# Optimization experiments

Measured on AMD Instinct MI355X. Metric: run time of the kernel, lower is better.

The kernel has to match this reference:

```python
import jax, jax.numpy as jnp
import numpy as np

N = 100000   # nodes
E = 1600000  # edges (avg degree 16)
F = 128      # num_features
H = 128      # hidden
BN_EPS = 1e-5
NORM_EPS = 1e-12


def setup_inputs() -> dict:
    key = jax.random.key(0)
    k = jax.random.split(key, 5)
    x = jax.random.normal(k[0], (N, F), dtype=jnp.float32)
    edge_index = jax.random.randint(k[1], (2, E), 0, N, dtype=jnp.int64)
    # Xavier-uniform linear weights (as in weights_init)
    s = float(np.sqrt(6.0 / (F + H)))
    W_l = jax.random.uniform(k[2], (F, H), jnp.float32, -s, s)  # neighbor branch
    b_l = jnp.zeros((H,), jnp.float32)
    W_r = jax.random.uniform(k[3], (F, H), jnp.float32, -s, s)  # root branch (no bias in PyG)
    gamma = jnp.ones((H,), jnp.float32)   # BatchNorm weight
    beta = jnp.zeros((H,), jnp.float32)   # BatchNorm bias
    return {"x": x, "edge_index": edge_index, "W_l": W_l, "b_l": b_l,
            "W_r": W_r, "gamma": gamma, "beta": beta}


def reference(x, edge_index, W_l, b_l, W_r, gamma, beta):
    n = x.shape[0]
    src, dst = edge_index[0], edge_index[1]
    # mean aggregation of neighbor messages x_j at destination nodes
    agg = jax.ops.segment_sum(x[src], dst, num_segments=n)                 # [N, F]
    deg = jax.ops.segment_sum(jnp.ones((src.shape[0],), x.dtype), dst,
                              num_segments=n)                              # [N]
    agg = agg / jnp.maximum(deg, 1.0)[:, None]
    # SAGEConv: lin_l(agg) + lin_r(x), then row-wise L2 normalize
    out = agg @ W_l + b_l + x @ W_r                                        # [N, H]
    nrm = jnp.sqrt(jnp.sum(out * out, axis=-1, keepdims=True))
    out = out / jnp.maximum(nrm, NORM_EPS)
    # transition: ReLU -> BatchNorm1d (batch stats, training mode) -> Dropout(identity)
    out = jax.nn.relu(out)
    mean = jnp.mean(out, axis=0)
    var = jnp.mean((out - mean) ** 2, axis=0)  # biased variance (torch BN)
    out = (out - mean) / jnp.sqrt(var + BN_EPS) * gamma + beta
    return out
```

## Files before the change

kernel.cpp:

```cpp
#include <hip/hip_runtime.h>
#include <hip/hip_bf16.h>

static constexpr int F = 128;
static constexpr int H = 128;
static constexpr int NPART = 128;

typedef __attribute__((ext_vector_type(8))) short short8;
typedef __attribute__((ext_vector_type(4))) float f32x4;

__device__ __forceinline__ unsigned short f2bf(float f) {
  union { float f; unsigned u; } a; a.f = f;
  unsigned r = a.u + 0x7FFF + ((a.u >> 16) & 1);
  return (unsigned short)(r >> 16);
}
__device__ __forceinline__ float bf2f(unsigned short h) {
  union { unsigned u; float f; } a; a.u = ((unsigned)h) << 16;
  return a.f;
}
__device__ __forceinline__ float bits2f(unsigned u) {
  union { unsigned u; float f; } a; a.u = u;
  return a.f;
}

__device__ __forceinline__ unsigned f2fp8(float f) {
  union { float f; unsigned u; } a; a.f = f;
  unsigned s = (a.u >> 24) & 0x80u;
  unsigned m = a.u & 0x7FFFFFFFu;
  if (m < 0x3C800000u) return s;
  unsigned r = m + 0x7FFFFu + ((m >> 20) & 1u);
  if (r > 0x43E00000u) r = 0x43E00000u;
  return s | ((((r >> 23) - 120u) & 15u) << 3) | ((r >> 20) & 7u);
}

__device__ __forceinline__ void fp8x4_to_f32(unsigned w, float& f0, float& f1,
                                             float& f2, float& f3) {
  unsigned lo = w & 0x00FF00FFu;
  unsigned hi = (w >> 8) & 0x00FF00FFu;
  unsigned p0 = (((lo << 4) & 0x07F007F0u) + 0x3C003C00u) | ((lo & 0x00800080u) << 8);
  unsigned p1 = (((hi << 4) & 0x07F007F0u) + 0x3C003C00u) | ((hi & 0x00800080u) << 8);
  f0 = bits2f(p0 << 16);
  f2 = bits2f(p0 & 0xFFFF0000u);
  f1 = bits2f(p1 << 16);
  f3 = bits2f(p1 & 0xFFFF0000u);
}

__device__ __forceinline__ int detect64(const void* eiv) {
  const unsigned* u = (const unsigned*)eiv;
  int is64 = 1;
  for (int i = 0; i < 64; ++i) is64 &= (u[2 * i + 1] == 0u);
  return is64;
}

__global__ void detect_dtype(const unsigned* __restrict__ ei, int* __restrict__ flag) {
  if (blockIdx.x == 0 && threadIdx.x == 0) {
    int is64 = 1;
    for (int i = 0; i < 64; ++i) {
      if (ei[2 * i + 1] != 0u) { is64 = 0; break; }
    }
    *flag = is64;
  }
}

__device__ __forceinline__ int load_idx(const void* eiv, int is64, long long pos) {
  return is64 ? (int)((const long long*)eiv)[pos] : ((const int*)eiv)[pos];
}

__global__ __launch_bounds__(512) void part_hist(const void* __restrict__ eiv,
                                                 int* __restrict__ cmat,
                                                 int E, int nbuck, int chunk) {
  __shared__ int h[2048];
  const int t = threadIdx.x, b = blockIdx.x;
  for (int i = t; i < nbuck; i += 512) h[i] = 0;
  __syncthreads();
  int is64 = detect64(eiv);
  int s = b * chunk, e = min(E, s + chunk);
  for (int i = s + t; i < e; i += 512) {
    int dst = load_idx(eiv, is64, (long long)E + i);
    atomicAdd(&h[dst >> 6], 1);
  }
  __syncthreads();
  for (int i = t; i < nbuck; i += 512) cmat[i * NPART + b] = h[i];
}

__global__ __launch_bounds__(256) void scan1(const int* __restrict__ in,
                                             int* __restrict__ outx,
                                             int* __restrict__ blocksum, int n) {
  __shared__ int sm[256];
  int idx = blockIdx.x * 256 + threadIdx.x;
  int v = (idx < n) ? in[idx] : 0;
  sm[threadIdx.x] = v;
  __syncthreads();
  #pragma unroll
  for (int off = 1; off < 256; off <<= 1) {
    int t = (threadIdx.x >= off) ? sm[threadIdx.x - off] : 0;
    __syncthreads();
    sm[threadIdx.x] += t;
    __syncthreads();
  }
  if (idx < n) outx[idx] = sm[threadIdx.x] - v;
  if (threadIdx.x == 255) blocksum[blockIdx.x] = sm[255];
}

__global__ __launch_bounds__(1024) void scan2big(const int* __restrict__ blocksum,
                                                 int* __restrict__ blockoff, int nb) {
  __shared__ int sm[1024];
  int t = threadIdx.x;
  int v = (t < nb) ? blocksum[t] : 0;
  sm[t] = v;
  __syncthreads();
  for (int off = 1; off < 1024; off <<= 1) {
    int u = (t >= off) ? sm[t - off] : 0;
    __syncthreads();
    sm[t] += u;
    __syncthreads();
  }
  if (t < nb) blockoff[t] = sm[t] - v;
}

__global__ __launch_bounds__(256) void scan3p(int* __restrict__ obuf,
                                              const int* __restrict__ blockoff,
                                              int* __restrict__ bbase,
                                              float* __restrict__ colzero,
                                              int L, int nbuck, int E) {
  if (blockIdx.x == 0) colzero[threadIdx.x] = 0.0f;
  int idx = blockIdx.x * 256 + threadIdx.x;
  if (idx >= L) return;
  int v = obuf[idx] + blockoff[idx >> 8];
  obuf[idx] = v;
  if ((idx & (NPART - 1)) == 0) bbase[idx / NPART] = v;
  if (idx == 0) bbase[nbuck] = E;
}

__global__ __launch_bounds__(512) void part_scatter(const void* __restrict__ eiv,
                                                    const int* __restrict__ base,
                                                    int* __restrict__ ebuf,
                                                    int E, int nbuck, int chunk) {
  __shared__ int cur[2048];
  const int t = threadIdx.x, b = blockIdx.x;
  for (int i = t; i < nbuck; i += 512) cur[i] = base[i * NPART + b];
  __syncthreads();
  int is64 = detect64(eiv);
  int s = b * chunk, e = min(E, s + chunk);
  for (int i = s + t; i < e; i += 512) {
    int src = load_idx(eiv, is64, i);
    int dst = load_idx(eiv, is64, (long long)E + i);
    int pos = atomicAdd(&cur[dst >> 6], 1);
    ebuf[pos] = (src << 6) | (dst & 63);
  }
}

#define GCAP 2048
template <bool LOWP>
__global__ __launch_bounds__(256) void gather_bucket(
    const unsigned char* __restrict__ Yf8, const int* __restrict__ ebuf,
    const int* __restrict__ bbase, float* __restrict__ pio,
    const unsigned short* __restrict__ Pbf, unsigned short* __restrict__ Ubf,
    float* __restrict__ colsum, float* __restrict__ colsq, int n) {
  __shared__ int lsrc[GCAP];
  __shared__ int hist[65];
  __shared__ int loff[65];
  __shared__ int cur[64];
  __shared__ float csm[128], cqm[128];

  const int t = threadIdx.x;
  const int b = blockIdx.x;
  const int node0 = b << 6;
  const int s = bbase[b], e = bbase[b + 1];
  const int cnt = e - s;

  if (t < 65) hist[t] = 0;
  if (t < 128) { csm[t] = 0.f; cqm[t] = 0.f; }
  __syncthreads();

  const bool fast = (cnt <= GCAP);
  if (fast) {
    for (int i = s + t; i < e; i += 256)
      atomicAdd(&hist[ebuf[i] & 63], 1);
    __syncthreads();
    if (t < 64) loff[t] = hist[t];
    __syncthreads();
    #pragma unroll
    for (int off = 1; off < 64; off <<= 1) {
      int u = (t >= off && t < 64) ? loff[t - off] : 0;
      __syncthreads();
      if (t < 64) loff[t] += u;
      __syncthreads();
    }
    if (t < 64) cur[t] = loff[t] - hist[t];
    __syncthreads();
    for (int i = s + t; i < e; i += 256) {
      int p = ebuf[i];
      int pos = atomicAdd(&cur[p & 63], 1);
      lsrc[pos] = p >> 6;
    }
    __syncthreads();
  }

  const int lane = t & 63;
  const int w = t >> 6;
  const int half = lane >> 5;
  const int c = (lane & 31) * 4;

  float lcs[4] = {0.f, 0.f, 0.f, 0.f};
  float lcq[4] = {0.f, 0.f, 0.f, 0.f};

  #pragma unroll
  for (int it = 0; it < 8; ++it) {
    int ln = it * 8 + w * 2 + half;
    int node = node0 + ln;
    if (node >= n) continue;
    int ls, le;
    if (fast) { ls = loff[ln] - hist[ln]; le = loff[ln]; }
    else      { ls = 0; le = 0; }

    float acc[8][4];
    #pragma unroll
    for (int u = 0; u < 8; ++u)
      #pragma unroll
      for (int q = 0; q < 4; ++q) acc[u][q] = 0.0f;

    int j = ls;
    for (; j + 7 < le; j += 8) {
      #pragma unroll
      for (int u = 0; u < 8; ++u) {
        int sj = lsrc[j + u];
        unsigned wv = *(const unsigned*)(Yf8 + (size_t)sj * H + c);
        float f0, f1, f2, f3;
        fp8x4_to_f32(wv, f0, f1, f2, f3);
        acc[u][0] += f0; acc[u][1] += f1; acc[u][2] += f2; acc[u][3] += f3;
      }
    }
    for (; j + 1 < le; j += 2) {
      #pragma unroll
      for (int u = 0; u < 2; ++u) {
        int sj = lsrc[j + u];
        unsigned wv = *(const unsigned*)(Yf8 + (size_t)sj * H + c);
        float f0, f1, f2, f3;
        fp8x4_to_f32(wv, f0, f1, f2, f3);
        acc[u][0] += f0; acc[u][1] += f1; acc[u][2] += f2; acc[u][3] += f3;
      }
    }
    if (j < le) {
      int sj = lsrc[j];
      unsigned wv = *(const unsigned*)(Yf8 + (size_t)sj * H + c);
      float f0, f1, f2, f3;
      fp8x4_to_f32(wv, f0, f1, f2, f3);
      acc[0][0] += f0; acc[0][1] += f1; acc[0][2] += f2; acc[0][3] += f3;
    }

    float deg = 0.0f;
    float a0, a1, a2, a3;
    if (fast) {
      deg = (float)(le - ls);
      #pragma unroll
      for (int u = 4; u < 8; ++u) {
        acc[u - 4][0] += acc[u][0]; acc[u - 4][1] += acc[u][1];
        acc[u - 4][2] += acc[u][2]; acc[u - 4][3] += acc[u][3];
      }
      a0 = (acc[0][0] + acc[1][0]) + (acc[2][0] + acc[3][0]);
      a1 = (acc[0][1] + acc[1][1]) + (acc[2][1] + acc[3][1]);
      a2 = (acc[0][2] + acc[1][2]) + (acc[2][2] + acc[3][2]);
      a3 = (acc[0][3] + acc[1][3]) + (acc[2][3] + acc[3][3]);
    } else {
      a0 = a1 = a2 = a3 = 0.0f;
      for (int jj = s; jj < e; ++jj) {
        int p = ebuf[jj];
        if ((p & 63) == ln) {
          deg += 1.0f;
          unsigned wv = *(const unsigned*)(Yf8 + (size_t)(p >> 6) * H + c);
          float f0, f1, f2, f3;
          fp8x4_to_f32(wv, f0, f1, f2, f3);
          a0 += f0; a1 += f1; a2 += f2; a3 += f3;
        }
      }
    }

    float inv = 1.0f / fmaxf(deg, 1.0f);
    float p0, p1, p2, p3;
    if (LOWP) {
      uint2 pv = *(const uint2*)(Pbf + (size_t)node * H + c);
      p0 = bits2f(pv.x << 16);
      p1 = bits2f(pv.x & 0xFFFF0000u);
      p2 = bits2f(pv.y << 16);
      p3 = bits2f(pv.y & 0xFFFF0000u);
    } else {
      float4 p = *(const float4*)(pio + (size_t)node * H + c);
      p0 = p.x; p1 = p.y; p2 = p.z; p3 = p.w;
    }
    float v0 = p0 + a0 * inv;
    float v1 = p1 + a1 * inv;
    float v2 = p2 + a2 * inv;
    float v3 = p3 + a3 * inv;
    float sq = v0 * v0 + v1 * v1 + v2 * v2 + v3 * v3;
    sq += __shfl_xor(sq, 1, 64);
    sq += __shfl_xor(sq, 2, 64);
    sq += __shfl_xor(sq, 4, 64);
    sq += __shfl_xor(sq, 8, 64);
    sq += __shfl_xor(sq, 16, 64);
    float rs = 1.0f / fmaxf(sqrtf(sq), 1e-12f);
    float u0 = fmaxf(v0 * rs, 0.f), u1 = fmaxf(v1 * rs, 0.f);
    float u2 = fmaxf(v2 * rs, 0.f), u3 = fmaxf(v3 * rs, 0.f);
    if (LOWP) {
      uint2 ov;
      ov.x = (unsigned)f2bf(u0) | ((unsigned)f2bf(u1) << 16);
      ov.y = (unsigned)f2bf(u2) | ((unsigned)f2bf(u3) << 16);
      *(uint2*)(Ubf + (size_t)node * H + c) = ov;
    } else {
      float4 o = {u0, u1, u2, u3};
      *(float4*)(pio + (size_t)node * H + c) = o;
    }
    lcs[0] += u0; lcq[0] += u0 * u0;
    lcs[1] += u1; lcq[1] += u1 * u1;
    lcs[2] += u2; lcq[2] += u2 * u2;
    lcs[3] += u3; lcq[3] += u3 * u3;
  }

  #pragma unroll
  for (int q = 0; q < 4; ++q) {
    atomicAdd(&csm[c + q], lcs[q]);
    atomicAdd(&cqm[c + q], lcq[q]);
  }
  __syncthreads();
  if (t < 128) {
    atomicAdd(&colsum[t], csm[t]);
    atomicAdd(&colsq[t], cqm[t]);
  }
}

__global__ __launch_bounds__(256) void deg_count(const void* __restrict__ eiv,
                                                 const int* __restrict__ flag,
                                                 int* __restrict__ degi, int E) {
  int e = blockIdx.x * blockDim.x + threadIdx.x;
  if (e >= E) return;
  int dst = load_idx(eiv, *flag, (long long)E + e);
  atomicAdd(&degi[dst], 1);
}

__global__ __launch_bounds__(256) void scan3(int* __restrict__ offsets,
                                             const int* __restrict__ blockoff,
                                             int* __restrict__ cursor, int n, int E) {
  int idx = blockIdx.x * 256 + threadIdx.x;
  if (idx >= n) return;
  int off = offsets[idx] + blockoff[idx >> 8];
  offsets[idx] = off;
  cursor[idx] = off;
  if (idx == 0) offsets[n] = E;
}

__global__ __launch_bounds__(256) void bucket_fill(const void* __restrict__ eiv,
                                                   const int* __restrict__ flag,
                                                   int* __restrict__ cursor,
                                                   int* __restrict__ csr_src, int E) {
  int e = blockIdx.x * blockDim.x + threadIdx.x;
  if (e >= E) return;
  int is64 = *flag;
  int src = load_idx(eiv, is64, e);
  int dst = load_idx(eiv, is64, (long long)E + e);
  int pos = atomicAdd(&cursor[dst], 1);
  csr_src[pos] = src;
}

__global__ __launch_bounds__(256) void prep_w(const float* __restrict__ Wl,
                                              const float* __restrict__ Wr,
                                              unsigned short* __restrict__ Wcat) {
  int tid = blockIdx.x * 256 + threadIdx.x;
  if (tid >= 4 * 4 * 8 * 64) return;
  int lane = tid & 63;
  int nf   = (tid >> 6) & 7;
  int kc   = (tid >> 9) & 3;
  int part = tid >> 11;
  const float* W = (part < 2) ? Wl : Wr;
  bool lo = (part & 1);
  int ncol = nf * 16 + (lane & 15);
  int k0 = kc * 32 + (lane >> 4) * 8;
  unsigned short ov[8];
  #pragma unroll
  for (int j = 0; j < 8; ++j) {
    float v = W[(k0 + j) * H + ncol];
    unsigned short h = f2bf(v);
    ov[j] = lo ? f2bf(v - bf2f(h)) : h;
  }
  uint4 pack;
  pack.x = (unsigned)ov[0] | ((unsigned)ov[1] << 16);
  pack.y = (unsigned)ov[2] | ((unsigned)ov[3] << 16);
  pack.z = (unsigned)ov[4] | ((unsigned)ov[5] << 16);
  pack.w = (unsigned)ov[6] | ((unsigned)ov[7] << 16);
  *(uint4*)(Wcat + (size_t)tid * 8) = pack;
}

template <bool LOWP>
__global__ __launch_bounds__(256) void dual_gemm(
    const float* __restrict__ x, const unsigned short* __restrict__ Wcat,
    const float* __restrict__ bl, unsigned char* __restrict__ Yf8,
    float* __restrict__ pout, unsigned short* __restrict__ Pbf, int n) {
  __shared__ unsigned short As[2][64][128];

  const int t = threadIdx.x;
  const int i0 = blockIdx.x * 64;

  #pragma unroll
  for (int it = 0; it < 8; ++it) {
    int idx = it * 256 + t;
    int r = idx >> 5;
    int c4 = (idx & 31) * 4;
    int row_g = i0 + r; if (row_g >= n) row_g = n - 1;
    int boff = (((c4 >> 3) ^ (r & 7)) << 3) + (c4 & 7);
    float4 vx = *(const float4*)(x + (size_t)row_g * F + c4);
    unsigned short h0 = f2bf(vx.x), h1 = f2bf(vx.y), h2 = f2bf(vx.z), h3 = f2bf(vx.w);
    uint2 hv = { (unsigned)h0 | ((unsigned)h1 << 16), (unsigned)h2 | ((unsigned)h3 << 16) };
    *(uint2*)&As[0][r][boff] = hv;
    unsigned short l0 = f2bf(vx.x - bf2f(h0)), l1 = f2bf(vx.y - bf2f(h1));
    unsigned short l2 = f2bf(vx.z - bf2f(h2)), l3 = f2bf(vx.w - bf2f(h3));
    uint2 lv = { (unsigned)l0 | ((unsigned)l1 << 16), (unsigned)l2 | ((unsigned)l3 << 16) };
    *(uint2*)&As[1][r][boff] = lv;
  }
  __syncthreads();

  const int w = t >> 6;
  const int lane = t & 63;

  f32x4 accL[4][2], accR[4][2];
  #pragma unroll
  for (int rf = 0; rf < 4; ++rf)
    #pragma unroll
    for (int nfi = 0; nfi < 2; ++nfi) {
      accL[rf][nfi] = (f32x4){0.f, 0.f, 0.f, 0.f};
      accR[rf][nfi] = (f32x4){0.f, 0.f, 0.f, 0.f};
    }

  const int APM[3] = {0, 1, 0};
  const int BL[3]  = {0, 0, 1};
  const int BR[3]  = {2, 2, 3};

  #pragma unroll
  for (int pass = 0; pass < 3; ++pass) {
    const int ap = APM[pass];
    #pragma unroll
    for (int kc = 0; kc < 4; ++kc) {
      short8 afr[4];
      int chunk = kc * 4 + (lane >> 4);
      #pragma unroll
      for (int rf = 0; rf < 4; ++rf) {
        int row = rf * 16 + (lane & 15);
        afr[rf] = *(const short8*)(&As[ap][row][(chunk ^ (row & 7)) * 8]);
      }
      short8 bfrL[2], bfrR[2];
      #pragma unroll
      for (int nfi = 0; nfi < 2; ++nfi) {
        int blobL = (BL[pass] * 4 + kc) * 8 + (w * 2 + nfi);
        int blobR = (BR[pass] * 4 + kc) * 8 + (w * 2 + nfi);
        bfrL[nfi] = *(const short8*)(Wcat + (size_t)blobL * 512 + lane * 8);
        bfrR[nfi] = *(const short8*)(Wcat + (size_t)blobR * 512 + lane * 8);
      }
      #pragma unroll
      for (int rf = 0; rf < 4; ++rf)
        #pragma unroll
        for (int nfi = 0; nfi < 2; ++nfi) {
          accL[rf][nfi] = __builtin_amdgcn_mfma_f32_16x16x32_bf16(
              afr[rf], bfrL[nfi], accL[rf][nfi], 0, 0, 0);
          accR[rf][nfi] = __builtin_amdgcn_mfma_f32_16x16x32_bf16(
              afr[rf], bfrR[nfi], accR[rf][nfi], 0, 0, 0);
        }
    }
  }

  const float b0 = bl[w * 32 + (lane & 15)];
  const float b1 = bl[w * 32 + 16 + (lane & 15)];

  #pragma unroll
  for (int rf = 0; rf < 4; ++rf) {
    #pragma unroll
    for (int r4 = 0; r4 < 4; ++r4) {
      int rl = rf * 16 + (lane >> 4) * 4 + r4;
      int row = i0 + rl;
      if (row < n) {
        Yf8[(size_t)row * H + w * 32 + (lane & 15)]      = (unsigned char)f2fp8(accL[rf][0][r4]);
        Yf8[(size_t)row * H + w * 32 + 16 + (lane & 15)] = (unsigned char)f2fp8(accL[rf][1][r4]);
        if (LOWP) {
          Pbf[(size_t)row * H + w * 32 + (lane & 15)]      = f2bf(accR[rf][0][r4] + b0);
          Pbf[(size_t)row * H + w * 32 + 16 + (lane & 15)] = f2bf(accR[rf][1][r4] + b1);
        } else {
          pout[(size_t)row * H + w * 32 + (lane & 15)]      = accR[rf][0][r4] + b0;
          pout[(size_t)row * H + w * 32 + 16 + (lane & 15)] = accR[rf][1][r4] + b1;
        }
      }
    }
  }
}

__global__ __launch_bounds__(256) void gather_mean(const float* __restrict__ x,
                                                   const int* __restrict__ offsets,
                                                   const int* __restrict__ csr_src,
                                                   float* __restrict__ out, int n) {
  int node = (int)(((long long)blockIdx.x * blockDim.x + threadIdx.x) >> 6);
  int lane = threadIdx.x & 63;
  if (node >= n) return;
  int s = offsets[node], e = offsets[node + 1];
  float ax = 0.0f, ay = 0.0f, bx = 0.0f, by = 0.0f;
  int j = s;
  for (; j + 1 < e; j += 2) {
    int s0 = csr_src[j], s1 = csr_src[j + 1];
    float2 v0 = *(const float2*)(x + (size_t)s0 * F + lane * 2);
    float2 v1 = *(const float2*)(x + (size_t)s1 * F + lane * 2);
    ax += v0.x; ay += v0.y;
    bx += v1.x; by += v1.y;
  }
  if (j < e) {
    int s0 = csr_src[j];
    float2 v0 = *(const float2*)(x + (size_t)s0 * F + lane * 2);
    ax += v0.x; ay += v0.y;
  }
  float inv = 1.0f / fmaxf((float)(e - s), 1.0f);
  float2 r; r.x = (ax + bx) * inv; r.y = (ay + by) * inv;
  *(float2*)(out + (size_t)node * H + lane * 2) = r;
}

__global__ __launch_bounds__(256) void mfma_gemm(
    const float* __restrict__ x, const unsigned short* __restrict__ Wcat,
    const float* __restrict__ bl, float* __restrict__ out,
    float* __restrict__ colsum, float* __restrict__ colsq, int n) {
  __shared__ unsigned short As[4][64][128];
  __shared__ float rowsq[64][4];
  __shared__ float rscale[64];

  const int t = threadIdx.x;
  const int i0 = blockIdx.x * 64;

  #pragma unroll
  for (int it = 0; it < 8; ++it) {
    int idx = it * 256 + t;
    int r = idx >> 5;
    int c4 = (idx & 31) * 4;
    int row_g = i0 + r; if (row_g >= n) row_g = n - 1;
    int boff = (((c4 >> 3) ^ (r & 7)) << 3) + (c4 & 7);
    float4 va = *(const float4*)(out + (size_t)row_g * H + c4);
    float4 vx = *(const float4*)(x + (size_t)row_g * H + c4);
    unsigned short h0 = f2bf(va.x), h1 = f2bf(va.y), h2 = f2bf(va.z), h3 = f2bf(va.w);
    uint2 hv = { (unsigned)h0 | ((unsigned)h1 << 16), (unsigned)h2 | ((unsigned)h3 << 16) };
    *(uint2*)&As[0][r][boff] = hv;
    unsigned short l0 = f2bf(va.x - bf2f(h0)), l1 = f2bf(va.y - bf2f(h1));
    unsigned short l2 = f2bf(va.z - bf2f(h2)), l3 = f2bf(va.w - bf2f(h3));
    uint2 lv = { (unsigned)l0 | ((unsigned)l1 << 16), (unsigned)l2 | ((unsigned)l3 << 16) };
    *(uint2*)&As[1][r][boff] = lv;
    h0 = f2bf(vx.x); h1 = f2bf(vx.y); h2 = f2bf(vx.z); h3 = f2bf(vx.w);
    uint2 hx = { (unsigned)h0 | ((unsigned)h1 << 16), (unsigned)h2 | ((unsigned)h3 << 16) };
    *(uint2*)&As[2][r][boff] = hx;
    l0 = f2bf(vx.x - bf2f(h0)); l1 = f2bf(vx.y - bf2f(h1));
    l2 = f2bf(vx.z - bf2f(h2)); l3 = f2bf(vx.w - bf2f(h3));
    uint2 lx = { (unsigned)l0 | ((unsigned)l1 << 16), (unsigned)l2 | ((unsigned)l3 << 16) };
    *(uint2*)&As[3][r][boff] = lx;
  }
  __syncthreads();

  const int w = t >> 6;
  const int lane = t & 63;

  f32x4 acc[4][2];
  #pragma unroll
  for (int rf = 0; rf < 4; ++rf)
    #pragma unroll
    for (int nfi = 0; nfi < 2; ++nfi)
      acc[rf][nfi] = (f32x4){0.f, 0.f, 0.f, 0.f};

  const int APM[6] = {0, 1, 0, 2, 3, 2};
  const int BPM[6] = {0, 0, 1, 2, 2, 3};

  #pragma unroll
  for (int pass = 0; pass < 6; ++pass) {
    const int ap = APM[pass], bp = BPM[pass];
    #pragma unroll
    for (int kc = 0; kc < 4; ++kc) {
      short8 bfr[2];
      #pragma unroll
      for (int nfi = 0; nfi < 2; ++nfi) {
        int blob = (bp * 4 + kc) * 8 + (w * 2 + nfi);
        bfr[nfi] = *(const short8*)(Wcat + (size_t)blob * 512 + lane * 8);
      }
      short8 afr[4];
      int chunk = kc * 4 + (lane >> 4);
      #pragma unroll
      for (int rf = 0; rf < 4; ++rf) {
        int row = rf * 16 + (lane & 15);
        afr[rf] = *(const short8*)(&As[ap][row][(chunk ^ (row & 7)) * 8]);
      }
      #pragma unroll
      for (int rf = 0; rf < 4; ++rf)
        #pragma unroll
        for (int nfi = 0; nfi < 2; ++nfi)
          acc[rf][nfi] = __builtin_amdgcn_mfma_f32_16x16x32_bf16(
              afr[rf], bfr[nfi], acc[rf][nfi], 0, 0, 0);
    }
  }

  const float b0 = bl[w * 32 + (lane & 15)];
  const float b1 = bl[w * 32 + 16 + (lane & 15)];

  #pragma unroll
  for (int rf = 0; rf < 4; ++rf) {
    #pragma unroll
    for (int r4 = 0; r4 < 4; ++r4) {
      float v0 = acc[rf][0][r4] + b0;
      float v1 = acc[rf][1][r4] + b1;
      acc[rf][0][r4] = v0;
      acc[rf][1][r4] = v1;
      float sq = v0 * v0 + v1 * v1;
      sq += __shfl_xor(sq, 1, 64);
      sq += __shfl_xor(sq, 2, 64);
      sq += __shfl_xor(sq, 4, 64);
      sq += __shfl_xor(sq, 8, 64);
      if ((lane & 15) == 0) rowsq[rf * 16 + (lane >> 4) * 4 + r4][w] = sq;
    }
  }
  __syncthreads();
  if (t < 64) {
    float s = rowsq[t][0] + rowsq[t][1] + rowsq[t][2] + rowsq[t][3];
    rscale[t] = 1.0f / fmaxf(sqrtf(s), 1e-12f);
  }
  __syncthreads();

  float cs0 = 0.f, cq0 = 0.f, cs1 = 0.f, cq1 = 0.f;
  #pragma unroll
  for (int rf = 0; rf < 4; ++rf) {
    #pragma unroll
    for (int r4 = 0; r4 < 4; ++r4) {
      int rl = rf * 16 + (lane >> 4) * 4 + r4;
      int row = i0 + rl;
      float s = rscale[rl];
      float u0 = fmaxf(acc[rf][0][r4] * s, 0.f);
      float u1 = fmaxf(acc[rf][1][r4] * s, 0.f);
      if (row < n) {
        out[(size_t)row * H + w * 32 + (lane & 15)] = u0;
        out[(size_t)row * H + w * 32 + 16 + (lane & 15)] = u1;
        cs0 += u0; cq0 += u0 * u0;
        cs1 += u1; cq1 += u1 * u1;
      }
    }
  }
  cs0 += __shfl_xor(cs0, 16, 64); cs0 += __shfl_xor(cs0, 32, 64);
  cq0 += __shfl_xor(cq0, 16, 64); cq0 += __shfl_xor(cq0, 32, 64);
  cs1 += __shfl_xor(cs1, 16, 64); cs1 += __shfl_xor(cs1, 32, 64);
  cq1 += __shfl_xor(cq1, 16, 64); cq1 += __shfl_xor(cq1, 32, 64);
  if (lane < 16) {
    atomicAdd(&colsum[w * 32 + lane], cs0);
    atomicAdd(&colsq[w * 32 + lane], cq0);
    atomicAdd(&colsum[w * 32 + 16 + lane], cs1);
    atomicAdd(&colsq[w * 32 + 16 + lane], cq1);
  }
}

__global__ __launch_bounds__(256) void scatter_mean(
    const float* __restrict__ x, const void* __restrict__ eiv,
    const int* __restrict__ flag, float* __restrict__ agg,
    float* __restrict__ deg, int E) {
  long long gid = (long long)blockIdx.x * blockDim.x + threadIdx.x;
  int e = (int)(gid >> 5);
  int ch = (int)(gid & 31);
  if (e >= E) return;
  int is64 = *flag;
  int src = load_idx(eiv, is64, e);
  int dst = load_idx(eiv, is64, (long long)E + e);
  float4 v = *(const float4*)(x + (size_t)src * F + ch * 4);
  float* a = agg + (size_t)dst * H + ch * 4;
  atomicAdd(a + 0, v.x);
  atomicAdd(a + 1, v.y);
  atomicAdd(a + 2, v.z);
  atomicAdd(a + 3, v.w);
  if (ch == 0) atomicAdd(deg + dst, 1.0f);
}

__global__ __launch_bounds__(256) void divide_deg(float* __restrict__ out,
                                                  const float* __restrict__ deg,
                                                  long long n4) {
  long long i = (long long)blockIdx.x * blockDim.x + threadIdx.x;
  if (i >= n4) return;
  int node = (int)(i >> 5);
  float s = 1.0f / fmaxf(deg[node], 1.0f);
  float4 v = ((float4*)out)[i];
  v.x *= s; v.y *= s; v.z *= s; v.w *= s;
  ((float4*)out)[i] = v;
}

__global__ __launch_bounds__(256) void fused_gemm(
    const float* __restrict__ x, const float* __restrict__ Wl,
    const float* __restrict__ bl, const float* __restrict__ Wr,
    float* __restrict__ out, float* __restrict__ colsum, float* __restrict__ colsq) {
  __shared__ float As[16][256];
  __shared__ float rp[4][8];
  __shared__ float rscale[16];
  __shared__ float cs[128], cs2[128];

  const int t = threadIdx.x;
  const int i0 = blockIdx.x * 16;

  #pragma unroll
  for (int it = 0; it < 2; ++it) {
    int idx = (it * 256 + t) * 4;
    int r = idx >> 7, c = idx & 127;
    float4 va = *(const float4*)(out + (size_t)(i0 + r) * H + c);
    As[r][c + 0] = va.x; As[r][c + 1] = va.y;
    As[r][c + 2] = va.z; As[r][c + 3] = va.w;
    float4 vx = *(const float4*)(x + (size_t)(i0 + r) * F + c);
    As[r][128 + c + 0] = vx.x; As[r][128 + c + 1] = vx.y;
    As[r][128 + c + 2] = vx.z; As[r][128 + c + 3] = vx.w;
  }
  __syncthreads();

  const int c = t & 127;
  const int half = t >> 7;
  float acc[8];
  #pragma unroll
  for (int r = 0; r < 8; ++r) acc[r] = 0.0f;

  #pragma unroll 4
  for (int k = 0; k < 128; ++k) {
    float w = Wl[k * H + c];
    #pragma unroll
    for (int r = 0; r < 8; ++r) acc[r] = fmaf(As[half * 8 + r][k], w, acc[r]);
  }
  #pragma unroll 4
  for (int k = 0; k < 128; ++k) {
    float w = Wr[k * H + c];
    #pragma unroll
    for (int r = 0; r < 8; ++r) acc[r] = fmaf(As[half * 8 + r][128 + k], w, acc[r]);
  }
  const float bias = bl[c];
  #pragma unroll
  for (int r = 0; r < 8; ++r) acc[r] += bias;

  float sq[8];
  #pragma unroll
  for (int r = 0; r < 8; ++r) sq[r] = acc[r] * acc[r];
  #pragma unroll
  for (int off = 32; off > 0; off >>= 1) {
    #pragma unroll
    for (int r = 0; r < 8; ++r) sq[r] += __shfl_down(sq[r], off, 64);
  }
  const int wv = t >> 6;
  if ((t & 63) == 0) {
    #pragma unroll
    for (int r = 0; r < 8; ++r) rp[wv][r] = sq[r];
  }
  __syncthreads();
  if (t < 16) {
    int base = (t >> 3) * 2, rr = t & 7;
    float s = rp[base][rr] + rp[base + 1][rr];
    rscale[t] = 1.0f / fmaxf(sqrtf(s), 1e-12f);
  }
  __syncthreads();

  float csum = 0.0f, csq = 0.0f;
  #pragma unroll
  for (int r = 0; r < 8; ++r) {
    float v = fmaxf(acc[r] * rscale[half * 8 + r], 0.0f);
    out[(size_t)(i0 + half * 8 + r) * H + c] = v;
    csum += v;
    csq += v * v;
  }
  if (half == 1) { cs[c] = csum; cs2[c] = csq; }
  __syncthreads();
  if (half == 0) {
    atomicAdd(&colsum[c], csum + cs[c]);
    atomicAdd(&colsq[c], csq + cs2[c]);
  }
}

__global__ void bn_stats(const float* __restrict__ colsum, const float* __restrict__ colsq,
                         const float* __restrict__ gamma, const float* __restrict__ beta,
                         float* __restrict__ scale, float* __restrict__ shift, int n) {
  int c = threadIdx.x;
  if (c < H) {
    float inv_n = 1.0f / (float)n;
    float mean = colsum[c] * inv_n;
    float var = colsq[c] * inv_n - mean * mean;
    float istd = rsqrtf(var + 1e-5f);
    float sc = gamma[c] * istd;
    scale[c] = sc;
    shift[c] = beta[c] - mean * sc;
  }
}

__global__ __launch_bounds__(256) void bn_apply(
    float* __restrict__ out, const float* __restrict__ scale,
    const float* __restrict__ shift, long long n4) {
  long long i = (long long)blockIdx.x * blockDim.x + threadIdx.x;
  if (i >= n4) return;
  float4 v = ((float4*)out)[i];
  int c = (int)((i * 4) & (H - 1));
  v.x = fmaf(v.x, scale[c + 0], shift[c + 0]);
  v.y = fmaf(v.y, scale[c + 1], shift[c + 1]);
  v.z = fmaf(v.z, scale[c + 2], shift[c + 2]);
  v.w = fmaf(v.w, scale[c + 3], shift[c + 3]);
  ((float4*)out)[i] = v;
}

__global__ __launch_bounds__(256) void bn_apply_lo(
    const unsigned short* __restrict__ U, float* __restrict__ out,
    const float* __restrict__ scale, const float* __restrict__ shift,
    long long n4) {
  long long i = (long long)blockIdx.x * blockDim.x + threadIdx.x;
  if (i >= n4) return;
  uint2 uv = ((const uint2*)U)[i];
  int c = (int)((i * 4) & (H - 1));
  float4 v;
  v.x = fmaf(bits2f(uv.x << 16),          scale[c + 0], shift[c + 0]);
  v.y = fmaf(bits2f(uv.x & 0xFFFF0000u),  scale[c + 1], shift[c + 1]);
  v.z = fmaf(bits2f(uv.y << 16),          scale[c + 2], shift[c + 2]);
  v.w = fmaf(bits2f(uv.y & 0xFFFF0000u),  scale[c + 3], shift[c + 3]);
  ((float4*)out)[i] = v;
}

extern "C" void kernel_launch(void* const* d_in, const int* in_sizes, int n_in,
                              void* d_out, int out_size, void* d_ws, size_t ws_size,
                              hipStream_t stream) {
  const float* x     = (const float*)d_in[0];
  const void*  ei    = d_in[1];
  const float* Wl    = (const float*)d_in[2];
  const float* bl    = (const float*)d_in[3];
  const float* Wr    = (const float*)d_in[4];
  const float* gamma = (const float*)d_in[5];
  const float* beta  = (const float*)d_in[6];
  float* out = (float*)d_out;

  const int n = in_sizes[0] / F;
  const int E = in_sizes[1] / 2;
  const int nb = (n + 255) / 256;
  const int nbuck = (n + 63) >> 6;

  char* ws = (char*)d_ws;
  int* flag = (int*)ws;
  unsigned short* Wcat = (unsigned short*)(ws + 256);
  char* after_w = ws + 256 + 4 * 128 * 128 * 2;

  int*   cmat    = (int*)after_w;
  int*   obuf    = cmat + 2048 * NPART;
  int*   bsum    = obuf + 2048 * NPART;
  int*   boff    = bsum + 1024;
  int*   bbase   = boff + 1024;
  float* fcs     = (float*)(bbase + 2049);
  float* fcq     = fcs + H;
  float* fsc     = fcq + H;
  float* fsh     = fsc + H;
  int*   ebuf    = (int*)(fsh + H);
  unsigned char*  Yf8 = (unsigned char*)(ebuf + E);
  unsigned short* Pws = (unsigned short*)(Yf8 + (size_t)n * H);
  unsigned short* Uws = Pws + (size_t)n * H;
  size_t need_fast  = (size_t)((char*)(Yf8 + (size_t)n * H) - ws);
  size_t need_fast2 = (size_t)((char*)(Uws + (size_t)n * H) - ws);

  int*   degi     = (int*)after_w;
  int*   offsets  = degi + n;
  int*   cursor   = offsets + n + 1;
  int*   blocksum = cursor + n;
  int*   blockoff = blocksum + nb;
  float* mcs      = (float*)(blockoff + nb);
  float* mcq      = mcs + H;
  float* msc      = mcq + H;
  float* msh      = msc + H;
  int*   csr_src  = (int*)(msh + H);
  size_t need_mid = (size_t)((char*)(csr_src + E) - ws);

  float *colsum, *colsq, *scale, *shift;

  const int eb = (E + 255) / 256;
  const int gb = (n + 63) / 64;
  const long long n4 = (long long)n * H / 4;

  if (ws_size >= need_fast && nbuck <= 2048) {
    const bool lowp = (ws_size >= need_fast2);
    colsum = fcs; colsq = fcq; scale = fsc; shift = fsh;

    prep_w<<<32, 256, 0, stream>>>(Wl, Wr, Wcat);
    if (lowp)
      dual_gemm<true><<<gb, 256, 0, stream>>>(x, Wcat, bl, Yf8, out, Pws, n);
    else
      dual_gemm<false><<<gb, 256, 0, stream>>>(x, Wcat, bl, Yf8, out, Pws, n);

    const int chunk = (E + NPART - 1) / NPART;
    const int L = nbuck * NPART;
    const int nb2 = (L + 255) / 256;
    part_hist<<<NPART, 512, 0, stream>>>(ei, cmat, E, nbuck, chunk);
    scan1<<<nb2, 256, 0, stream>>>(cmat, obuf, bsum, L);
    scan2big<<<1, 1024, 0, stream>>>(bsum, boff, nb2);
    scan3p<<<nb2, 256, 0, stream>>>(obuf, boff, bbase, colsum, L, nbuck, E);
    part_scatter<<<NPART, 512, 0, stream>>>(ei, obuf, ebuf, E, nbuck, chunk);

    if (lowp)
      gather_bucket<true><<<nbuck, 256, 0, stream>>>(
          Yf8, ebuf, bbase, out, Pws, Uws, colsum, colsq, n);
    else
      gather_bucket<false><<<nbuck, 256, 0, stream>>>(
          Yf8, ebuf, bbase, out, Pws, Uws, colsum, colsq, n);

    bn_stats<<<1, 128, 0, stream>>>(colsum, colsq, gamma, beta, scale, shift, n);
    if (lowp)
      bn_apply_lo<<<(int)((n4 + 255) / 256), 256, 0, stream>>>(
          Uws, out, scale, shift, n4);
    else
      bn_apply<<<(int)((n4 + 255) / 256), 256, 0, stream>>>(out, scale, shift, n4);
  } else if (ws_size >= need_mid) {
    colsum = mcs; colsq = mcq; scale = msc; shift = msh;
    detect_dtype<<<1, 64, 0, stream>>>((const unsigned*)ei, flag);
    hipMemsetAsync(degi, 0, (size_t)n * 4, stream);
    hipMemsetAsync(colsum, 0, 2 * H * 4, stream);

    prep_w<<<32, 256, 0, stream>>>(Wl, Wr, Wcat);

    deg_count<<<eb, 256, 0, stream>>>(ei, flag, degi, E);
    scan1<<<nb, 256, 0, stream>>>(degi, offsets, blocksum, n);
    scan2big<<<1, 1024, 0, stream>>>(blocksum, blockoff, nb);
    scan3<<<nb, 256, 0, stream>>>(offsets, blockoff, cursor, n, E);
    bucket_fill<<<eb, 256, 0, stream>>>(ei, flag, cursor, csr_src, E);

    long long gthreads = (long long)n * 64;
    gather_mean<<<(int)((gthreads + 255) / 256), 256, 0, stream>>>(
        x, offsets, csr_src, out, n);

    mfma_gemm<<<gb, 256, 0, stream>>>(x, Wcat, bl, out, colsum, colsq, n);
    bn_stats<<<1, 128, 0, stream>>>(colsum, colsq, gamma, beta, scale, shift, n);
    bn_apply<<<(int)((n4 + 255) / 256), 256, 0, stream>>>(out, scale, shift, n4);
  } else {
    float* deg = (float*)(ws + 256);
    colsum = deg + n; colsq = colsum + H; scale = colsq + H; shift = scale + H;
    detect_dtype<<<1, 64, 0, stream>>>((const unsigned*)ei, flag);
    hipMemsetAsync(d_out, 0, (size_t)out_size * sizeof(float), stream);
    hipMemsetAsync(deg, 0, (size_t)n * 4 + 4 * H * 4, stream);
    long long sthreads = (long long)E * 32;
    scatter_mean<<<(int)((sthreads + 255) / 256), 256, 0, stream>>>(x, ei, flag, out, deg, E);
    long long n4f = (long long)n * H / 4;
    divide_deg<<<(int)((n4f + 255) / 256), 256, 0, stream>>>(out, deg, n4f);
    fused_gemm<<<n / 16, 256, 0, stream>>>(x, Wl, bl, Wr, out, colsum, colsq);
    bn_stats<<<1, 128, 0, stream>>>(colsum, colsq, gamma, beta, scale, shift, n);
    bn_apply<<<(int)((n4 + 255) / 256), 256, 0, stream>>>(out, scale, shift, n4);
  }
}
```

Measured before the change: 203.8 us.

## Fuse edge histogram into dual GEMM launch and accumulate gathers in packed fp16

Merges the per-partition destination histogram kernel into the dual GEMM launch: the first NPART blocks build the histogram in the GEMM's shared memory and the rest do the GEMM. Both run in one grid, which removes a launch and lets the memory-bound histogram overlap the MFMA work. The gather loop also now decodes fp8 straight to packed half2 and accumulates with packed fp16 adds instead of four fp32 accumulators, cutting ALU and register use. The risk is lost precision or overflow when summing in fp16 for high-degree nodes.

```diff
diff --git a/kernel.cpp b/kernel.cpp
--- a/kernel.cpp
+++ b/kernel.cpp
@@ -7,6 +7,7 @@
 
 typedef __attribute__((ext_vector_type(8))) short short8;
 typedef __attribute__((ext_vector_type(4))) float f32x4;
+typedef __attribute__((ext_vector_type(2))) _Float16 h2v;
 
 __device__ __forceinline__ unsigned short f2bf(float f) {
   union { float f; unsigned u; } a; a.f = f;
@@ -20,6 +21,9 @@
 __device__ __forceinline__ float bits2f(unsigned u) {
   union { unsigned u; float f; } a; a.u = u;
   return a.f;
+}
+__device__ __forceinline__ h2v bits2h2(unsigned u) {
+  union { unsigned u; h2v h; } a; a.u = u; return a.h;
 }
 
 __device__ __forceinline__ unsigned f2fp8(float f) {
@@ -30,6 +34,15 @@
   unsigned r = m + 0x7FFFFu + ((m >> 20) & 1u);
   if (r > 0x43E00000u) r = 0x43E00000u;
   return s | ((((r >> 23) - 120u) & 15u) << 3) | ((r >> 20) & 7u);
+}
+
+__device__ __forceinline__ void fp8x4_to_h2(unsigned w, h2v& p02, h2v& p13) {
+  unsigned lo = w & 0x00FF00FFu;
+  unsigned hi = (w >> 8) & 0x00FF00FFu;
+  unsigned q0 = (((lo << 7) & 0x3F803F80u) + 0x20002000u) | ((lo & 0x00800080u) << 8);
+  unsigned q1 = (((hi << 7) & 0x3F803F80u) + 0x20002000u) | ((hi & 0x00800080u) << 8);
+  p02 = bits2h2(q0);
+  p13 = bits2h2(q1);
 }
 
 __device__ __forceinline__ void fp8x4_to_f32(unsigned w, float& f0, float& f1,
@@ -63,23 +76,6 @@
 
 __device__ __forceinline__ int load_idx(const void* eiv, int is64, long long pos) {
   return is64 ? (int)((const long long*)eiv)[pos] : ((const int*)eiv)[pos];
-}
-
-__global__ __launch_bounds__(512) void part_hist(const void* __restrict__ eiv,
-                                                 int* __restrict__ cmat,
-                                                 int E, int nbuck, int chunk) {
-  __shared__ int h[2048];
-  const int t = threadIdx.x, b = blockIdx.x;
-  for (int i = t; i < nbuck; i += 512) h[i] = 0;
-  __syncthreads();
-  int is64 = detect64(eiv);
-  int s = b * chunk, e = min(E, s + chunk);
-  for (int i = s + t; i < e; i += 512) {
-    int dst = load_idx(eiv, is64, (long long)E + i);
-    atomicAdd(&h[dst >> 6], 1);
-  }
-  __syncthreads();
-  for (int i = t; i < nbuck; i += 512) cmat[i * NPART + b] = h[i];
 }
 
 __global__ __launch_bounds__(256) void scan1(const int* __restrict__ in,
@@ -149,6 +145,153 @@
   }
 }
 
+__global__ __launch_bounds__(256) void prep_w(const float* __restrict__ Wl,
+                                              const float* __restrict__ Wr,
+                                              unsigned short* __restrict__ Wcat) {
+  int tid = blockIdx.x * 256 + threadIdx.x;
+  if (tid >= 4 * 4 * 8 * 64) return;
+  int lane = tid & 63;
+  int nf   = (tid >> 6) & 7;
+  int kc   = (tid >> 9) & 3;
+  int part = tid >> 11;
+  const float* W = (part < 2) ? Wl : Wr;
+  bool lo = (part & 1);
+  int ncol = nf * 16 + (lane & 15);
+  int k0 = kc * 32 + (lane >> 4) * 8;
+  unsigned short ov[8];
+  #pragma unroll
+  for (int j = 0; j < 8; ++j) {
+    float v = W[(k0 + j) * H + ncol];
+    unsigned short h = f2bf(v);
+    ov[j] = lo ? f2bf(v - bf2f(h)) : h;
+  }
+  uint4 pack;
+  pack.x = (unsigned)ov[0] | ((unsigned)ov[1] << 16);
+  pack.y = (unsigned)ov[2] | ((unsigned)ov[3] << 16);
+  pack.z = (unsigned)ov[4] | ((unsigned)ov[5] << 16);
+  pack.w = (unsigned)ov[6] | ((unsigned)ov[7] << 16);
+  *(uint4*)(Wcat + (size_t)tid * 8) = pack;
+}
+
+template <bool LOWP>
+__global__ __launch_bounds__(256) void fused_gemm_hist(
+    const float* __restrict__ x, const unsigned short* __restrict__ Wcat,
+    const float* __restrict__ bl, unsigned char* __restrict__ Yf8,
+    float* __restrict__ pout, unsigned short* __restrict__ Pbf, int n,
+    const void* __restrict__ eiv, int* __restrict__ cmat, int E, int nbuck,
+    int chunk) {
+  __shared__ unsigned short As[2][64][128];
+
+  const int t = threadIdx.x;
+
+  if (blockIdx.x < NPART) {
+    int* h = (int*)&As[0][0][0];
+    const int b = blockIdx.x;
+    for (int i = t; i < nbuck; i += 256) h[i] = 0;
+    __syncthreads();
+    int is64 = detect64(eiv);
+    int s = b * chunk, e = min(E, s + chunk);
+    for (int i = s + t; i < e; i += 256) {
+      int dst = load_idx(eiv, is64, (long long)E + i);
+      atomicAdd(&h[dst >> 6], 1);
+    }
+    __syncthreads();
+    for (int i = t; i < nbuck; i += 256) cmat[i * NPART + b] = h[i];
+    return;
+  }
+
+  const int i0 = (blockIdx.x - NPART) * 64;
+
+  #pragma unroll
+  for (int it = 0; it < 8; ++it) {
+    int idx = it * 256 + t;
+    int r = idx >> 5;
+    int c4 = (idx & 31) * 4;
+    int row_g = i0 + r; if (row_g >= n) row_g = n - 1;
+    int boff = (((c4 >> 3) ^ (r & 7)) << 3) + (c4 & 7);
+    float4 vx = *(const float4*)(x + (size_t)row_g * F + c4);
+    unsigned short h0 = f2bf(vx.x), h1 = f2bf(vx.y), h2 = f2bf(vx.z), h3 = f2bf(vx.w);
+    uint2 hv = { (unsigned)h0 | ((unsigned)h1 << 16), (unsigned)h2 | ((unsigned)h3 << 16) };
+    *(uint2*)&As[0][r][boff] = hv;
+    unsigned short l0 = f2bf(vx.x - bf2f(h0)), l1 = f2bf(vx.y - bf2f(h1));
+    unsigned short l2 = f2bf(vx.z - bf2f(h2)), l3 = f2bf(vx.w - bf2f(h3));
+    uint2 lv = { (unsigned)l0 | ((unsigned)l1 << 16), (unsigned)l2 | ((unsigned)l3 << 16) };
+    *(uint2*)&As[1][r][boff] = lv;
+  }
+  __syncthreads();
+
+  const int w = t >> 6;
+  const int lane = t & 63;
+
+  f32x4 accL[4][2], accR[4][2];
+  #pragma unroll
+  for (int rf = 0; rf < 4; ++rf)
+    #pragma unroll
+    for (int nfi = 0; nfi < 2; ++nfi) {
+      accL[rf][nfi] = (f32x4){0.f, 0.f, 0.f, 0.f};
+      accR[rf][nfi] = (f32x4){0.f, 0.f, 0.f, 0.f};
+    }
+
+  const int APM[3] = {0, 1, 0};
+  const int BL[3]  = {0, 0, 1};
+  const int BR[3]  = {2, 2, 3};
+
+  #pragma unroll
+  for (int pass = 0; pass < 3; ++pass) {
+    const int ap = APM[pass];
+    #pragma unroll
+    for (int kc = 0; kc < 4; ++kc) {
+      short8 afr[4];
+      int chunk2 = kc * 4 + (lane >> 4);
+      #pragma unroll
+      for (int rf = 0; rf < 4; ++rf) {
+        int row = rf * 16 + (lane & 15);
+        afr[rf] = *(const short8*)(&As[ap][row][(chunk2 ^ (row & 7)) * 8]);
+      }
+      short8 bfrL[2], bfrR[2];
+      #pragma unroll
+      for (int nfi = 0; nfi < 2; ++nfi) {
+        int blobL = (BL[pass] * 4 + kc) * 8 + (w * 2 + nfi);
+        int blobR = (BR[pass] * 4 + kc) * 8 + (w * 2 + nfi);
+        bfrL[nfi] = *(const short8*)(Wcat + (size_t)blobL * 512 + lane * 8);
+        bfrR[nfi] = *(const short8*)(Wcat + (size_t)blobR * 512 + lane * 8);
+      }
+      #pragma unroll
+      for (int rf = 0; rf < 4; ++rf)
+        #pragma unroll
+        for (int nfi = 0; nfi < 2; ++nfi) {
+          accL[rf][nfi] = __builtin_amdgcn_mfma_f32_16x16x32_bf16(
+              afr[rf], bfrL[nfi], accL[rf][nfi], 0, 0, 0);
+          accR[rf][nfi] = __builtin_amdgcn_mfma_f32_16x16x32_bf16(
+              afr[rf], bfrR[nfi], accR[rf][nfi], 0, 0, 0);
+        }
+    }
+  }
+
+  const float b0 = bl[w * 32 + (lane & 15)];
+  const float b1 = bl[w * 32 + 16 + (lane & 15)];
+
+  #pragma unroll
+  for (int rf = 0; rf < 4; ++rf) {
+    #pragma unroll
+    for (int r4 = 0; r4 < 4; ++r4) {
+      int rl = rf * 16 + (lane >> 4) * 4 + r4;
+      int row = i0 + rl;
+      if (row < n) {
+        Yf8[(size_t)row * H + w * 32 + (lane & 15)]      = (unsigned char)f2fp8(accL[rf][0][r4]);
+        Yf8[(size_t)row * H + w * 32 + 16 + (lane & 15)] = (unsigned char)f2fp8(accL[rf][1][r4]);
+        if (LOWP) {
+          Pbf[(size_t)row * H + w * 32 + (lane & 15)]      = f2bf(accR[rf][0][r4] + b0);
+          Pbf[(size_t)row * H + w * 32 + 16 + (lane & 15)] = f2bf(accR[rf][1][r4] + b1);
+        } else {
+          pout[(size_t)row * H + w * 32 + (lane & 15)]      = accR[rf][0][r4] + b0;
+          pout[(size_t)row * H + w * 32 + 16 + (lane & 15)] = accR[rf][1][r4] + b1;
+        }
+      }
+    }
+  }
+}
+
 #define GCAP 2048
 template <bool LOWP>
 __global__ __launch_bounds__(256) void gather_bucket(
@@ -213,11 +356,12 @@
     if (fast) { ls = loff[ln] - hist[ln]; le = loff[ln]; }
     else      { ls = 0; le = 0; }
 
-    float acc[8][4];
-    #pragma unroll
-    for (int u = 0; u < 8; ++u)
-      #pragma unroll
-      for (int q = 0; q < 4; ++q) acc[u][q] = 0.0f;
+    h2v a02[8], a13[8];
+    #pragma unroll
+    for (int u = 0; u < 8; ++u) {
+      a02[u] = (h2v)(_Float16)0;
+      a13[u] = (h2v)(_Float16)0;
+    }
 
     int j = ls;
     for (; j + 7 < le; j += 8) {
@@ -225,9 +369,10 @@
       for (int u = 0; u < 8; ++u) {
         int sj = lsrc[j + u];
         unsigned wv = *(const unsigned*)(Yf8 + (size_t)sj * H + c);
-        float f0, f1, f2, f3;
-        fp8x4_to_f32(wv, f0, f1, f2, f3);
-        acc[u][0] += f0; acc[u][1] += f1; acc[u][2] += f2; acc[u][3] += f3;
+        h2v p02, p13;
+        fp8x4_to_h2(wv, p02, p13);
+        a02[u] += p02;
+        a13[u] += p13;
       }
     }
     for (; j + 1 < le; j += 2) {
@@ -235,32 +380,31 @@
       for (int u = 0; u < 2; ++u) {
         int sj = lsrc[j + u];
         unsigned wv = *(const unsigned*)(Yf8 + (size_t)sj * H + c);
-        float f0, f1, f2, f3;
-        fp8x4_to_f32(wv, f0, f1, f2, f3);
-        acc[u][0] += f0; acc[u][1] += f1; acc[u][2] += f2; acc[u][3] += f3;
+        h2v p02, p13;
+        fp8x4_to_h2(wv, p02, p13);
+        a02[u] += p02;
+        a13[u] += p13;
       }
     }
     if (j < le) {
       int sj = lsrc[j];
       unsigned wv = *(const unsigned*)(Yf8 + (size_t)sj * H + c);
-      float f0, f1, f2, f3;
-      fp8x4_to_f32(wv, f0, f1, f2, f3);
-      acc[0][0] += f0; acc[0][1] += f1; acc[0][2] += f2; acc[0][3] += f3;
+      h2v p02, p13;
+      fp8x4_to_h2(wv, p02, p13);
+      a02[0] += p02;
+      a13[0] += p13;
     }
 
     float deg = 0.0f;
     float a0, a1, a2, a3;
     if (fast) {
       deg = (float)(le - ls);
-      #pragma unroll
-      for (int u = 4; u < 8; ++u) {
-        acc[u - 4][0] += acc[u][0]; acc[u - 4][1] += acc[u][1];
-        acc[u - 4][2] += acc[u][2]; acc[u - 4][3] += acc[u][3];
-      }
-      a0 = (acc[0][0] + acc[1][0]) + (acc[2][0] + acc[3][0]);
-      a1 = (acc[0][1] + acc[1][1]) + (acc[2][1] + acc[3][1]);
-      a2 = (acc[0][2] + acc[1][2]) + (acc[2][2] + acc[3][2]);
-      a3 = (acc[0][3] + acc[1][3]) + (acc[2][3] + acc[3][3]);
+      h2v s02 = ((a02[0] + a02[1]) + (a02[2] + a02[3])) +
+                ((a02[4] + a02[5]) + (a02[6] + a02[7]));
+      h2v s13 = ((a13[0] + a13[1]) + (a13[2] + a13[3])) +
+                ((a13[4] + a13[5]) + (a13[6] + a13[7]));
+      a0 = (float)s02[0]; a2 = (float)s02[1];
+      a1 = (float)s13[0]; a3 = (float)s13[1];
     } else {
       a0 = a1 = a2 = a3 = 0.0f;
       for (int jj = s; jj < e; ++jj) {
@@ -358,134 +502,6 @@
   int dst = load_idx(eiv, is64, (long long)E + e);
   int pos = atomicAdd(&cursor[dst], 1);
   csr_src[pos] = src;
-}
-
-__global__ __launch_bounds__(256) void prep_w(const float* __restrict__ Wl,
-                                              const float* __restrict__ Wr,
-                                              unsigned short* __restrict__ Wcat) {
-  int tid = blockIdx.x * 256 + threadIdx.x;
-  if (tid >= 4 * 4 * 8 * 64) return;
-  int lane = tid & 63;
-  int nf   = (tid >> 6) & 7;
-  int kc   = (tid >> 9) & 3;
-  int part = tid >> 11;
-  const float* W = (part < 2) ? Wl : Wr;
-  bool lo = (part & 1);
-  int ncol = nf * 16 + (lane & 15);
-  int k0 = kc * 32 + (lane >> 4) * 8;
-  unsigned short ov[8];
-  #pragma unroll
-  for (int j = 0; j < 8; ++j) {
-    float v = W[(k0 + j) * H + ncol];
-    unsigned short h = f2bf(v);
-    ov[j] = lo ? f2bf(v - bf2f(h)) : h;
-  }
-  uint4 pack;
-  pack.x = (unsigned)ov[0] | ((unsigned)ov[1] << 16);
-  pack.y = (unsigned)ov[2] | ((unsigned)ov[3] << 16);
-  pack.z = (unsigned)ov[4] | ((unsigned)ov[5] << 16);
-  pack.w = (unsigned)ov[6] | ((unsigned)ov[7] << 16);
-  *(uint4*)(Wcat + (size_t)tid * 8) = pack;
-}
-
-template <bool LOWP>
-__global__ __launch_bounds__(256) void dual_gemm(
-    const float* __restrict__ x, const unsigned short* __restrict__ Wcat,
-    const float* __restrict__ bl, unsigned char* __restrict__ Yf8,
-    float* __restrict__ pout, unsigned short* __restrict__ Pbf, int n) {
-  __shared__ unsigned short As[2][64][128];
-
-  const int t = threadIdx.x;
-  const int i0 = blockIdx.x * 64;
-
-  #pragma unroll
-  for (int it = 0; it < 8; ++it) {
-    int idx = it * 256 + t;
-    int r = idx >> 5;
-    int c4 = (idx & 31) * 4;
-    int row_g = i0 + r; if (row_g >= n) row_g = n - 1;
-    int boff = (((c4 >> 3) ^ (r & 7)) << 3) + (c4 & 7);
-    float4 vx = *(const float4*)(x + (size_t)row_g * F + c4);
-    unsigned short h0 = f2bf(vx.x), h1 = f2bf(vx.y), h2 = f2bf(vx.z), h3 = f2bf(vx.w);
-    uint2 hv = { (unsigned)h0 | ((unsigned)h1 << 16), (unsigned)h2 | ((unsigned)h3 << 16) };
-    *(uint2*)&As[0][r][boff] = hv;
-    unsigned short l0 = f2bf(vx.x - bf2f(h0)), l1 = f2bf(vx.y - bf2f(h1));
-    unsigned short l2 = f2bf(vx.z - bf2f(h2)), l3 = f2bf(vx.w - bf2f(h3));
-    uint2 lv = { (unsigned)l0 | ((unsigned)l1 << 16), (unsigned)l2 | ((unsigned)l3 << 16) };
-    *(uint2*)&As[1][r][boff] = lv;
-  }
-  __syncthreads();
-
-  const int w = t >> 6;
-  const int lane = t & 63;
-
-  f32x4 accL[4][2], accR[4][2];
-  #pragma unroll
-  for (int rf = 0; rf < 4; ++rf)
-    #pragma unroll
-    for (int nfi = 0; nfi < 2; ++nfi) {
-      accL[rf][nfi] = (f32x4){0.f, 0.f, 0.f, 0.f};
-      accR[rf][nfi] = (f32x4){0.f, 0.f, 0.f, 0.f};
-    }
-
-  const int APM[3] = {0, 1, 0};
-  const int BL[3]  = {0, 0, 1};
-  const int BR[3]  = {2, 2, 3};
-
-  #pragma unroll
-  for (int pass = 0; pass < 3; ++pass) {
-    const int ap = APM[pass];
-    #pragma unroll
-    for (int kc = 0; kc < 4; ++kc) {
-      short8 afr[4];
-      int chunk = kc * 4 + (lane >> 4);
-      #pragma unroll
-      for (int rf = 0; rf < 4; ++rf) {
-        int row = rf * 16 + (lane & 15);
-        afr[rf] = *(const short8*)(&As[ap][row][(chunk ^ (row & 7)) * 8]);
-      }
-      short8 bfrL[2], bfrR[2];
-      #pragma unroll
-      for (int nfi = 0; nfi < 2; ++nfi) {
-        int blobL = (BL[pass] * 4 + kc) * 8 + (w * 2 + nfi);
-        int blobR = (BR[pass] * 4 + kc) * 8 + (w * 2 + nfi);
-        bfrL[nfi] = *(const short8*)(Wcat + (size_t)blobL * 512 + lane * 8);
-        bfrR[nfi] = *(const short8*)(Wcat + (size_t)blobR * 512 + lane * 8);
-      }
-      #pragma unroll
-      for (int rf = 0; rf < 4; ++rf)
-        #pragma unroll
-        for (int nfi = 0; nfi < 2; ++nfi) {
-          accL[rf][nfi] = __builtin_amdgcn_mfma_f32_16x16x32_bf16(
-              afr[rf], bfrL[nfi], accL[rf][nfi], 0, 0, 0);
-          accR[rf][nfi] = __builtin_amdgcn_mfma_f32_16x16x32_bf16(
-              afr[rf], bfrR[nfi], accR[rf][nfi], 0, 0, 0);
-        }
-    }
-  }
-
-  const float b0 = bl[w * 32 + (lane & 15)];
-  const float b1 = bl[w * 32 + 16 + (lane & 15)];
-
-  #pragma unroll
-  for (int rf = 0; rf < 4; ++rf) {
-    #pragma unroll
-    for (int r4 = 0; r4 < 4; ++r4) {
-      int rl = rf * 16 + (lane >> 4) * 4 + r4;
-      int row = i0 + rl;
-      if (row < n) {
-        Yf8[(size_t)row * H + w * 32 + (lane & 15)]      = (unsigned char)f2fp8(accL[rf][0][r4]);
-        Yf8[(size_t)row * H + w * 32 + 16 + (lane & 15)] = (unsigned char)f2fp8(accL[rf][1][r4]);
-        if (LOWP) {
-          Pbf[(size_t)row * H + w * 32 + (lane & 15)]      = f2bf(accR[rf][0][r4] + b0);
-          Pbf[(size_t)row * H + w * 32 + 16 + (lane & 15)] = f2bf(accR[rf][1][r4] + b1);
-        } else {
-          pout[(size_t)row * H + w * 32 + (lane & 15)]      = accR[rf][0][r4] + b0;
-          pout[(size_t)row * H + w * 32 + 16 + (lane & 15)] = accR[rf][1][r4] + b1;
-        }
-      }
-    }
-  }
 }
 
 __global__ __launch_bounds__(256) void gather_mean(const float* __restrict__ x,
@@ -869,16 +885,18 @@
     const bool lowp = (ws_size >= need_fast2);
     colsum = fcs; colsq = fcq; scale = fsc; shift = fsh;
 
-    prep_w<<<32, 256, 0, stream>>>(Wl, Wr, Wcat);
-    if (lowp)
-      dual_gemm<true><<<gb, 256, 0, stream>>>(x, Wcat, bl, Yf8, out, Pws, n);
-    else
-      dual_gemm<false><<<gb, 256, 0, stream>>>(x, Wcat, bl, Yf8, out, Pws, n);
-
     const int chunk = (E + NPART - 1) / NPART;
     const int L = nbuck * NPART;
     const int nb2 = (L + 255) / 256;
-    part_hist<<<NPART, 512, 0, stream>>>(ei, cmat, E, nbuck, chunk);
+
+    prep_w<<<32, 256, 0, stream>>>(Wl, Wr, Wcat);
+    if (lowp)
+      fused_gemm_hist<true><<<NPART + gb, 256, 0, stream>>>(
+          x, Wcat, bl, Yf8, out, Pws, n, ei, cmat, E, nbuck, chunk);
+    else
+      fused_gemm_hist<false><<<NPART + gb, 256, 0, stream>>>(
+          x, Wcat, bl, Yf8, out, Pws, n, ei, cmat, E, nbuck, chunk);
+
     scan1<<<nb2, 256, 0, stream>>>(cmat, obuf, bsum, L);
     scan2big<<<1, 1024, 0, stream>>>(bsum, boff, nb2);
     scan3p<<<nb2, 256, 0, stream>>>(obuf, boff, bbase, colsum, L, nbuck, E);
```

Result: faster. 190.6 us (-6.5%).
